# Kernel tuning notes

Hardware: AMD Instinct MI355X
Metric: run time of the kernel (lower is better)

The kernel has to match this reference:

```python
import jax, jax.numpy as jnp
import numpy as np

NUM_HEADS = 12
D = 768
HD = D // NUM_HEADS  # 64

def setup_inputs() -> dict:
    key = jax.random.key(0)
    ks = jax.random.split(key, 9)
    s = 0.02
    return {
        "x": jax.random.normal(ks[0], (4, 2048, D), dtype=jnp.float32),
        "QW_w": jax.random.normal(ks[1], (D, D), dtype=jnp.float32) * s,
        "QW_b": jax.random.normal(ks[2], (D,), dtype=jnp.float32) * s,
        "KW_w": jax.random.normal(ks[3], (D, D), dtype=jnp.float32) * s,
        "KW_b": jax.random.normal(ks[4], (D,), dtype=jnp.float32) * s,
        "VW_w": jax.random.normal(ks[5], (D, D), dtype=jnp.float32) * s,
        "VW_b": jax.random.normal(ks[6], (D,), dtype=jnp.float32) * s,
        "OW_w": jax.random.normal(ks[7], (D, D), dtype=jnp.float32) * s,
        "OW_b": jax.random.normal(ks[8], (D,), dtype=jnp.float32) * s,
    }

def reference(x, QW_w, QW_b, KW_w, KW_b, VW_w, VW_b, OW_w, OW_b):
    b, s, _ = x.shape
    # torch nn.Linear: y = x @ W.T + b
    def proj(w, bias):
        y = jnp.einsum('bsd,ed->bse', x, w) + bias
        return y.reshape(b, s, NUM_HEADS, HD).transpose(0, 2, 1, 3)  # [b,h,s,hd]
    q = proj(QW_w, QW_b)
    k = proj(KW_w, KW_b)
    v = proj(VW_w, VW_b)
    scores = jnp.einsum('bhqd,bhkd->bhqk', q, k) / jnp.sqrt(jnp.float32(HD))
    attn = jax.nn.softmax(scores, axis=-1)
    out = jnp.einsum('bhqk,bhkd->bhqd', attn, v)
    out = out.transpose(0, 2, 1, 3).reshape(b, s, NUM_HEADS * HD)
    return jnp.einsum('bsd,ed->bse', out, OW_w) + OW_b
```

## Files before the change

kernel.cpp:

```cpp
#include <hip/hip_runtime.h>
#include <hip/hip_bf16.h>

#define NH  12
#define HD  64
#define DIM 768
#define SEQ 2048
#define NB  4
#define MM  (NB*SEQ)
#define NKB (SEQ/64)

typedef short    v8s  __attribute__((ext_vector_type(8)));
typedef float    v4f  __attribute__((ext_vector_type(4)));
typedef float    v16f __attribute__((ext_vector_type(16)));
typedef unsigned v4u  __attribute__((ext_vector_type(4)));

#if __has_builtin(__builtin_amdgcn_exp2f)
#define EXP2(x) __builtin_amdgcn_exp2f(x)
#else
#define EXP2(x) __builtin_exp2f(x)
#endif

static __device__ __forceinline__ unsigned short f2b(float f) {
    unsigned int u = __float_as_uint(f);
    return (unsigned short)((u + 0x7FFFu + ((u >> 16) & 1u)) >> 16);
}
static __device__ __forceinline__ unsigned pk2bf(float lo, float hi) {
    return __builtin_amdgcn_perm(__float_as_uint(hi) + 0x8000u,
                                 __float_as_uint(lo) + 0x8000u, 0x07060302u);
}
static __device__ __forceinline__ void g2l16(const unsigned short* g, unsigned short* l) {
    __builtin_amdgcn_global_load_lds(
        (const __attribute__((address_space(1))) void*)g,
        (__attribute__((address_space(3))) void*)l, 16, 0, 0);
}

__global__ void cast_f32_bf16(const float* __restrict__ in,
                              unsigned short* __restrict__ out, int n4) {
    int i = blockIdx.x * blockDim.x + threadIdx.x;
    if (i < n4) {
        float4 v = reinterpret_cast<const float4*>(in)[i];
        ushort4 o;
        o.x = f2b(v.x); o.y = f2b(v.y); o.z = f2b(v.z); o.w = f2b(v.w);
        reinterpret_cast<ushort4*>(out)[i] = o;
    }
}

__global__ void cast4_f32_bf16(const float* __restrict__ i0, const float* __restrict__ i1,
                               const float* __restrict__ i2, const float* __restrict__ i3,
                               unsigned short* __restrict__ o0, unsigned short* __restrict__ o1,
                               unsigned short* __restrict__ o2, unsigned short* __restrict__ o3,
                               int n4) {
    int i = blockIdx.x * blockDim.x + threadIdx.x;
    if (i >= n4) return;
    const float* in; unsigned short* out;
    switch (blockIdx.y) {
        case 0: in = i0; out = o0; break;
        case 1: in = i1; out = o1; break;
        case 2: in = i2; out = o2; break;
        default: in = i3; out = o3; break;
    }
    float4 v = reinterpret_cast<const float4*>(in)[i];
    ushort4 o;
    o.x = f2b(v.x); o.y = f2b(v.y); o.z = f2b(v.z); o.w = f2b(v.w);
    reinterpret_cast<ushort4*>(out)[i] = o;
}

__global__ __launch_bounds__(256, 3) void gemm_qkv(
    const unsigned short* __restrict__ A,
    const unsigned short* __restrict__ Wq,
    const unsigned short* __restrict__ Wk,
    const unsigned short* __restrict__ Wv,
    const float* __restrict__ bq,
    const float* __restrict__ bk,
    const float* __restrict__ bvp,
    unsigned short* __restrict__ Qb,
    unsigned short* __restrict__ Kb,
    unsigned short* __restrict__ Vf)
{
    __shared__ __align__(16) unsigned short As[128 * 64];
    __shared__ __align__(16) unsigned short Bs[3][64 * 64];

    const int tid  = threadIdx.x;
    const int w    = tid >> 6, lane = tid & 63;
    const int quad = lane >> 4, l16 = lane & 15;
    const int wm   = w & 1,  wn = w >> 1;
    const int lane8 = lane >> 3, sc = lane & 7;
    const int m0   = blockIdx.x * 128;
    const int h    = blockIdx.y;
    const int n0   = h * 64;

    v4f acc[3][4][2];
    #pragma unroll
    for (int s = 0; s < 3; ++s)
        #pragma unroll
        for (int i = 0; i < 4; ++i)
            #pragma unroll
            for (int j = 0; j < 2; ++j)
                acc[s][i][j] = v4f{0.f, 0.f, 0.f, 0.f};

    for (int kb = 0; kb < DIM; kb += 64) {
        __syncthreads();
        #pragma unroll
        for (int t = 0; t < 4; ++t) {
            int r8 = w * 32 + t * 8;
            int r  = r8 + lane8;
            int gch = sc ^ (r & 7);
            g2l16(&A[(size_t)(m0 + r) * DIM + kb + gch * 8], &As[r8 * 64]);
        }
        #pragma unroll
        for (int u = 0; u < 6; ++u) {
            int G = w * 6 + u;
            int set = G >> 3, rg = G & 7;
            int row = rg * 8 + lane8;
            int gch = sc ^ (row & 7);
            const unsigned short* Wp = (set == 0) ? Wq : (set == 1) ? Wk : Wv;
            g2l16(&Wp[(size_t)(n0 + row) * DIM + kb + gch * 8], &Bs[set][rg * 8 * 64]);
        }
        __syncthreads();
        #pragma unroll
        for (int kk = 0; kk < 64; kk += 32) {
            int chb = kk >> 3;
            v8s a[4];
            #pragma unroll
            for (int i = 0; i < 4; ++i) {
                int m = wm * 64 + i * 16 + l16;
                a[i] = *reinterpret_cast<const v8s*>(
                    &As[m * 64 + (((chb + quad) ^ (m & 7)) << 3)]);
            }
            #pragma unroll
            for (int s = 0; s < 3; ++s) {
                v8s b[2];
                #pragma unroll
                for (int j = 0; j < 2; ++j) {
                    int n = wn * 32 + j * 16 + l16;
                    b[j] = *reinterpret_cast<const v8s*>(
                        &Bs[s][n * 64 + (((chb + quad) ^ (n & 7)) << 3)]);
                }
                #pragma unroll
                for (int i = 0; i < 4; ++i)
                    #pragma unroll
                    for (int j = 0; j < 2; ++j)
                        acc[s][i][j] = __builtin_amdgcn_mfma_f32_16x16x32_bf16(
                            a[i], b[j], acc[s][i][j], 0, 0, 0);
            }
        }
    }

    #pragma unroll
    for (int s = 0; s < 2; ++s) {
        unsigned short* out = s ? Kb : Qb;
        const float* bias   = s ? bk : bq;
        const float scale   = s ? 1.0f : 0.1803368801f;
        #pragma unroll
        for (int i = 0; i < 4; ++i) {
            #pragma unroll
            for (int j = 0; j < 2; ++j) {
                int hd = wn * 32 + j * 16 + l16;
                float bias_v = bias[n0 + hd];
                #pragma unroll
                for (int r = 0; r < 4; ++r) {
                    int gm = m0 + wm * 64 + i * 16 + quad * 4 + r;
                    int bb = gm >> 11, sq = gm & (SEQ - 1);
                    out[((size_t)(bb * NH + h) * SEQ + sq) * HD + hd] =
                        f2b((acc[s][i][j][r] + bias_v) * scale);
                }
            }
        }
    }
    #pragma unroll
    for (int i = 0; i < 4; ++i) {
        #pragma unroll
        for (int j = 0; j < 2; ++j) {
            int hd = wn * 32 + j * 16 + l16;
            int hb = hd >> 5, l31v = hd & 31;
            float bias_v = bvp[n0 + hd];
            int gm0 = m0 + wm * 64 + i * 16 + quad * 4;
            int bb = gm0 >> 11, sk = gm0 & (SEQ - 1);
            int kbi = sk >> 6;
            int halfv = quad >> 1, j0 = (quad & 1) * 4;
            ushort4 pkv;
            pkv.x = f2b(acc[2][i][j][0] + bias_v);
            pkv.y = f2b(acc[2][i][j][1] + bias_v);
            pkv.z = f2b(acc[2][i][j][2] + bias_v);
            pkv.w = f2b(acc[2][i][j][3] + bias_v);
            size_t frag = ((size_t)(bb * NH + h) * NKB + kbi) * 8 + hb * 4 + i;
            *reinterpret_cast<ushort4*>(
                &Vf[frag * 512 + (halfv * 32 + l31v) * 8 + j0]) = pkv;
        }
    }
}

__global__ __launch_bounds__(256, 3) void gemm_o(
    const unsigned short* __restrict__ A,
    const unsigned short* __restrict__ W,
    const float* __restrict__ bias,
    float* __restrict__ out)
{
    __shared__ __align__(16) unsigned short As[128 * 64];
    __shared__ __align__(16) unsigned short Bs[64 * 64];

    const int tid  = threadIdx.x;
    const int w    = tid >> 6, lane = tid & 63;
    const int quad = lane >> 4, l16 = lane & 15;
    const int wm   = w & 1,  wn = w >> 1;
    const int lane8 = lane >> 3, sc = lane & 7;
    const int m0  = blockIdx.x * 128;
    const int n0l = blockIdx.y * 64;

    v4f acc[4][2];
    #pragma unroll
    for (int i = 0; i < 4; ++i)
        #pragma unroll
        for (int j = 0; j < 2; ++j)
            acc[i][j] = v4f{0.f, 0.f, 0.f, 0.f};

    for (int kb = 0; kb < DIM; kb += 64) {
        __syncthreads();
        #pragma unroll
        for (int t = 0; t < 4; ++t) {
            int r8 = w * 32 + t * 8;
            int r  = r8 + lane8;
            int gch = sc ^ (r & 7);
            g2l16(&A[(size_t)(m0 + r) * DIM + kb + gch * 8], &As[r8 * 64]);
        }
        #pragma unroll
        for (int t = 0; t < 2; ++t) {
            int r8 = (w * 2 + t) * 8;
            int r  = r8 + lane8;
            int gch = sc ^ (r & 7);
            g2l16(&W[(size_t)(n0l + r) * DIM + kb + gch * 8], &Bs[r8 * 64]);
        }
        __syncthreads();
        #pragma unroll
        for (int kk = 0; kk < 64; kk += 32) {
            v8s a[4], b[2];
            int chb = kk >> 3;
            #pragma unroll
            for (int i = 0; i < 4; ++i) {
                int m = wm * 64 + i * 16 + l16;
                a[i] = *reinterpret_cast<const v8s*>(
                    &As[m * 64 + (((chb + quad) ^ (m & 7)) << 3)]);
            }
            #pragma unroll
            for (int j = 0; j < 2; ++j) {
                int n = wn * 32 + j * 16 + l16;
                b[j] = *reinterpret_cast<const v8s*>(
                    &Bs[n * 64 + (((chb + quad) ^ (n & 7)) << 3)]);
            }
            #pragma unroll
            for (int i = 0; i < 4; ++i)
                #pragma unroll
                for (int j = 0; j < 2; ++j)
                    acc[i][j] = __builtin_amdgcn_mfma_f32_16x16x32_bf16(a[i], b[j], acc[i][j], 0, 0, 0);
        }
    }

    #pragma unroll
    for (int i = 0; i < 4; ++i) {
        #pragma unroll
        for (int j = 0; j < 2; ++j) {
            int gn = n0l + wn * 32 + j * 16 + l16;
            float bias_v = bias[gn];
            #pragma unroll
            for (int r = 0; r < 4; ++r) {
                int gm = m0 + wm * 64 + i * 16 + quad * 4 + r;
                out[(size_t)gm * DIM + gn] = acc[i][j][r] + bias_v;
            }
        }
    }
}

__global__ __launch_bounds__(256, 3) void attn(
    const unsigned short* __restrict__ Q,
    const unsigned short* __restrict__ K,
    const unsigned short* __restrict__ Vf,
    unsigned short* __restrict__ ctx)
{
    __shared__ __align__(16) unsigned short Ks[2][64 * 64];

    const int tid  = threadIdx.x;
    const int w    = tid >> 6, lane = tid & 63;
    const int l31  = lane & 31, half = lane >> 5;
    const int lane8 = lane >> 3, sc = lane & 7;
    const int bh   = blockIdx.y;
    const int b    = bh / NH, h = bh % NH;
    const int q0   = blockIdx.x * 128 + w * 32;

    const unsigned short* Qp = Q  + ((size_t)bh * SEQ + q0) * HD;
    const unsigned short* Kp = K  + (size_t)bh * SEQ * HD;
    const unsigned short* Vh = Vf + (size_t)bh * NKB * 8 * 512 + lane * 8;

    v8s bq[4];
    #pragma unroll
    for (int c = 0; c < 4; ++c)
        bq[c] = *reinterpret_cast<const v8s*>(&Qp[l31 * HD + c * 16 + half * 8]);

    v8s va[2][4];
    #pragma unroll
    for (int hb = 0; hb < 2; ++hb)
        #pragma unroll
        for (int c = 0; c < 4; ++c)
            va[hb][c] = *reinterpret_cast<const v8s*>(&Vh[(hb * 4 + c) * 512]);

    v16f o0, o1, Z;
    #pragma unroll
    for (int i = 0; i < 16; ++i) { o0[i] = 0.f; o1[i] = 0.f; Z[i] = 0.f; }
    float li = 0.f;

    const int rx = l31 & 7;
    int rdoff[4];
    #pragma unroll
    for (int c = 0; c < 4; ++c)
        rdoff[c] = l31 * 64 + (((c * 2 + half) ^ rx) << 3);

    #define STAGE_K(kb_, buf_)                                                       \
        do {                                                                         \
            _Pragma("unroll")                                                        \
            for (int t = 0; t < 2; ++t) {                                            \
                int r8  = (t * 4 + w) * 8;                                           \
                int row = r8 + lane8;                                                \
                int gch = sc ^ (row & 7);                                            \
                g2l16(&Kp[(size_t)((kb_) + row) * HD + gch * 8], &Ks[buf_][r8 * 64]);\
            }                                                                        \
        } while (0)

    STAGE_K(0, 0);

    for (int it = 0; it < NKB; ++it) {
        const int buf = it & 1;
        __syncthreads();
        if (it + 1 < NKB) STAGE_K((it + 1) * 64, buf ^ 1);

        v16f s0, s1;
        {
            v8s ka00 = *reinterpret_cast<const v8s*>(&Ks[buf][rdoff[0]]);
            v8s ka10 = *reinterpret_cast<const v8s*>(&Ks[buf][rdoff[0] + 2048]);
            s0 = __builtin_amdgcn_mfma_f32_32x32x16_bf16(ka00, bq[0], Z, 0, 0, 0);
            s1 = __builtin_amdgcn_mfma_f32_32x32x16_bf16(ka10, bq[0], Z, 0, 0, 0);
            #pragma unroll
            for (int c = 1; c < 4; ++c) {
                v8s k0 = *reinterpret_cast<const v8s*>(&Ks[buf][rdoff[c]]);
                v8s k1 = *reinterpret_cast<const v8s*>(&Ks[buf][rdoff[c] + 2048]);
                s0 = __builtin_amdgcn_mfma_f32_32x32x16_bf16(k0, bq[c], s0, 0, 0, 0);
                s1 = __builtin_amdgcn_mfma_f32_32x32x16_bf16(k1, bq[c], s1, 0, 0, 0);
            }
        }

        unsigned pk[8][2];
        #pragma unroll
        for (int g = 0; g < 4; ++g) {
            float e0 = EXP2(s0[4*g+0]), e1 = EXP2(s0[4*g+1]);
            float e2 = EXP2(s0[4*g+2]), e3 = EXP2(s0[4*g+3]);
            li += (e0 + e1) + (e2 + e3);
            pk[g][0] = pk2bf(e0, e1);
            pk[g][1] = pk2bf(e2, e3);
            float f0 = EXP2(s1[4*g+0]), f1 = EXP2(s1[4*g+1]);
            float f2 = EXP2(s1[4*g+2]), f3 = EXP2(s1[4*g+3]);
            li += (f0 + f1) + (f2 + f3);
            pk[4+g][0] = pk2bf(f0, f1);
            pk[4+g][1] = pk2bf(f2, f3);
        }

        #pragma unroll
        for (int cp = 0; cp < 4; ++cp) {
            unsigned a0 = pk[2*cp][0],   a1 = pk[2*cp][1];
            unsigned b0 = pk[2*cp+1][0], b1 = pk[2*cp+1][1];
            unsigned u0 = half ? a0 : b0;
            unsigned u1 = half ? a1 : b1;
            unsigned x0 = __shfl_xor(u0, 32);
            unsigned x1 = __shfl_xor(u1, 32);
            v4u fw;
            fw.x = half ? x0 : a0;
            fw.y = half ? x1 : a1;
            fw.z = half ? b0 : x0;
            fw.w = half ? b1 : x1;
            v8s pf = __builtin_bit_cast(v8s, fw);
            o0 = __builtin_amdgcn_mfma_f32_32x32x16_bf16(va[0][cp], pf, o0, 0, 0, 0);
            o1 = __builtin_amdgcn_mfma_f32_32x32x16_bf16(va[1][cp], pf, o1, 0, 0, 0);
        }

        if (it + 1 < NKB) {
            const unsigned short* Vn = Vh + (size_t)(it + 1) * 8 * 512;
            #pragma unroll
            for (int hb = 0; hb < 2; ++hb)
                #pragma unroll
                for (int c = 0; c < 4; ++c)
                    va[hb][c] = *reinterpret_cast<const v8s*>(&Vn[(hb * 4 + c) * 512]);
        }
    }
    #undef STAGE_K

    float inv = 1.0f / (li + __shfl_xor(li, 32));

    const int q = q0 + l31;
    size_t base = ((size_t)(b * SEQ + q)) * DIM + h * HD;
    #pragma unroll
    for (int g = 0; g < 4; ++g) {
        int hd0 = 8 * g + 4 * half;
        uint2 u0, u1;
        u0.x = pk2bf(o0[4*g+0] * inv, o0[4*g+1] * inv);
        u0.y = pk2bf(o0[4*g+2] * inv, o0[4*g+3] * inv);
        u1.x = pk2bf(o1[4*g+0] * inv, o1[4*g+1] * inv);
        u1.y = pk2bf(o1[4*g+2] * inv, o1[4*g+3] * inv);
        *reinterpret_cast<uint2*>(&ctx[base + hd0])      = u0;
        *reinterpret_cast<uint2*>(&ctx[base + 32 + hd0]) = u1;
    }
}

extern "C" void kernel_launch(void* const* d_in, const int* in_sizes, int n_in,
                              void* d_out, int out_size, void* d_ws, size_t ws_size,
                              hipStream_t stream) {
    const float* x  = (const float*)d_in[0];
    const float* qw = (const float*)d_in[1]; const float* qb = (const float*)d_in[2];
    const float* kw = (const float*)d_in[3]; const float* kb = (const float*)d_in[4];
    const float* vw = (const float*)d_in[5]; const float* vb = (const float*)d_in[6];
    const float* ow = (const float*)d_in[7]; const float* ob = (const float*)d_in[8];
    float* out = (float*)d_out;

    char* ws = (char*)d_ws;
    size_t off = 0;
    auto alloc = [&](size_t bytes) -> unsigned short* {
        unsigned short* p = (unsigned short*)(ws + off);
        off += (bytes + 255) & ~(size_t)255;
        return p;
    };
    const size_t XB = (size_t)MM * DIM * 2;
    const size_t WB = (size_t)DIM * DIM * 2;
    const size_t QB = (size_t)NB * NH * SEQ * HD * 2;

    unsigned short* xb  = alloc(XB);
    unsigned short* wqb = alloc(WB);
    unsigned short* wkb = alloc(WB);
    unsigned short* wvb = alloc(WB);
    unsigned short* wob = alloc(WB);
    unsigned short* Qb  = alloc(QB);
    unsigned short* Kb  = alloc(QB);
    unsigned short* Vfb = alloc(QB);
    unsigned short* ctx = alloc(XB);

    const int n4x = MM * DIM / 4;
    const int n4w = DIM * DIM / 4;
    cast_f32_bf16<<<(n4x + 255) / 256, 256, 0, stream>>>(x, xb, n4x);
    cast4_f32_bf16<<<dim3((n4w + 255) / 256, 4), 256, 0, stream>>>(
        qw, kw, vw, ow, wqb, wkb, wvb, wob, n4w);

    gemm_qkv<<<dim3(MM / 128, NH), 256, 0, stream>>>(
        xb, wqb, wkb, wvb, qb, kb, vb, Qb, Kb, Vfb);

    attn<<<dim3(SEQ / 128, NB * NH), 256, 0, stream>>>(Qb, Kb, Vfb, ctx);

    gemm_o<<<dim3(MM / 128, DIM / 64), 256, 0, stream>>>(ctx, wob, ob, out);
}
```

Before: 210.8 us.

## Store K in MFMA fragment layout and load K directly to registers

The QKV GEMM now writes K in a pre-swizzled per-64-key-block fragment layout, the same way V is stored. The attention kernel then loads K fragments straight from global memory into registers, prefetching one block ahead, instead of staging K through double-buffered LDS with __syncthreads. This removes the LDS traffic and barriers from the attention loop, at the cost of more register pressure and every wave reading K from global/L2 on its own. The packed bf16 conversion also switches from a manual perm trick to the hardware v_cvt_pk_bf16_f32 instruction.

```diff
diff --git a/kernel.cpp b/kernel.cpp
--- a/kernel.cpp
+++ b/kernel.cpp
@@ -24,9 +24,10 @@
     unsigned int u = __float_as_uint(f);
     return (unsigned short)((u + 0x7FFFu + ((u >> 16) & 1u)) >> 16);
 }
-static __device__ __forceinline__ unsigned pk2bf(float lo, float hi) {
-    return __builtin_amdgcn_perm(__float_as_uint(hi) + 0x8000u,
-                                 __float_as_uint(lo) + 0x8000u, 0x07060302u);
+static __device__ __forceinline__ unsigned cvtpk(float lo, float hi) {
+    unsigned r;
+    asm("v_cvt_pk_bf16_f32 %0, %1, %2" : "=v"(r) : "v"(lo), "v"(hi));
+    return r;
 }
 static __device__ __forceinline__ void g2l16(const unsigned short* g, unsigned short* l) {
     __builtin_amdgcn_global_load_lds(
@@ -74,7 +75,7 @@
     const float* __restrict__ bk,
     const float* __restrict__ bvp,
     unsigned short* __restrict__ Qb,
-    unsigned short* __restrict__ Kb,
+    unsigned short* __restrict__ Kfo,
     unsigned short* __restrict__ Vf)
 {
     __shared__ __align__(16) unsigned short As[128 * 64];
@@ -147,24 +148,39 @@
     }
 
     #pragma unroll
-    for (int s = 0; s < 2; ++s) {
-        unsigned short* out = s ? Kb : Qb;
-        const float* bias   = s ? bk : bq;
-        const float scale   = s ? 1.0f : 0.1803368801f;
-        #pragma unroll
-        for (int i = 0; i < 4; ++i) {
-            #pragma unroll
-            for (int j = 0; j < 2; ++j) {
-                int hd = wn * 32 + j * 16 + l16;
-                float bias_v = bias[n0 + hd];
-                #pragma unroll
-                for (int r = 0; r < 4; ++r) {
-                    int gm = m0 + wm * 64 + i * 16 + quad * 4 + r;
-                    int bb = gm >> 11, sq = gm & (SEQ - 1);
-                    out[((size_t)(bb * NH + h) * SEQ + sq) * HD + hd] =
-                        f2b((acc[s][i][j][r] + bias_v) * scale);
-                }
-            }
+    for (int i = 0; i < 4; ++i) {
+        #pragma unroll
+        for (int j = 0; j < 2; ++j) {
+            int hd = wn * 32 + j * 16 + l16;
+            float bias_v = bq[n0 + hd];
+            #pragma unroll
+            for (int r = 0; r < 4; ++r) {
+                int gm = m0 + wm * 64 + i * 16 + quad * 4 + r;
+                int bb = gm >> 11, sq = gm & (SEQ - 1);
+                Qb[((size_t)(bb * NH + h) * SEQ + sq) * HD + hd] =
+                    f2b((acc[0][i][j][r] + bias_v) * 0.1803368801f);
+            }
+        }
+    }
+    #pragma unroll
+    for (int i = 0; i < 4; ++i) {
+        int kh = i >> 1;
+        #pragma unroll
+        for (int j = 0; j < 2; ++j) {
+            int hd = wn * 32 + j * 16 + l16;
+            int c  = hd >> 4;
+            int half_a = (l16 >> 3) & 1;
+            int jj = l16 & 7;
+            float bias_v = bk[n0 + hd];
+            int gm0 = m0 + wm * 64 + i * 16 + quad * 4;
+            int bb = gm0 >> 11, sk = gm0 & (SEQ - 1);
+            int t = sk >> 6;
+            int l31k = (i & 1) * 16 + quad * 4;
+            size_t frag = ((size_t)(bb * NH + h) * NKB + t) * 8 + kh * 4 + c;
+            unsigned short* dst = &Kfo[frag * 512 + (half_a * 32 + l31k) * 8 + jj];
+            #pragma unroll
+            for (int r = 0; r < 4; ++r)
+                dst[r * 8] = f2b(acc[1][i][j][r] + bias_v);
         }
     }
     #pragma unroll
@@ -272,78 +288,53 @@
 
 __global__ __launch_bounds__(256, 3) void attn(
     const unsigned short* __restrict__ Q,
-    const unsigned short* __restrict__ K,
+    const unsigned short* __restrict__ Kf,
     const unsigned short* __restrict__ Vf,
     unsigned short* __restrict__ ctx)
 {
-    __shared__ __align__(16) unsigned short Ks[2][64 * 64];
-
     const int tid  = threadIdx.x;
     const int w    = tid >> 6, lane = tid & 63;
     const int l31  = lane & 31, half = lane >> 5;
-    const int lane8 = lane >> 3, sc = lane & 7;
     const int bh   = blockIdx.y;
     const int b    = bh / NH, h = bh % NH;
     const int q0   = blockIdx.x * 128 + w * 32;
 
     const unsigned short* Qp = Q  + ((size_t)bh * SEQ + q0) * HD;
-    const unsigned short* Kp = K  + (size_t)bh * SEQ * HD;
-    const unsigned short* Vh = Vf + (size_t)bh * NKB * 8 * 512 + lane * 8;
+    const unsigned short* Vh = Vf + (size_t)bh * (NKB * 8 * 512) + lane * 8;
+    const unsigned short* Kh = Kf + (size_t)bh * (NKB * 8 * 512) + lane * 8;
 
     v8s bq[4];
     #pragma unroll
     for (int c = 0; c < 4; ++c)
         bq[c] = *reinterpret_cast<const v8s*>(&Qp[l31 * HD + c * 16 + half * 8]);
 
-    v8s va[2][4];
-    #pragma unroll
-    for (int hb = 0; hb < 2; ++hb)
-        #pragma unroll
-        for (int c = 0; c < 4; ++c)
-            va[hb][c] = *reinterpret_cast<const v8s*>(&Vh[(hb * 4 + c) * 512]);
+    v8s ka[2][4], va[2][4];
+    #pragma unroll
+    for (int g = 0; g < 8; ++g)
+        reinterpret_cast<v8s*>(ka)[g] = *reinterpret_cast<const v8s*>(&Kh[g * 512]);
+    #pragma unroll
+    for (int g = 0; g < 8; ++g)
+        reinterpret_cast<v8s*>(va)[g] = *reinterpret_cast<const v8s*>(&Vh[g * 512]);
 
     v16f o0, o1, Z;
     #pragma unroll
     for (int i = 0; i < 16; ++i) { o0[i] = 0.f; o1[i] = 0.f; Z[i] = 0.f; }
     float li = 0.f;
 
-    const int rx = l31 & 7;
-    int rdoff[4];
-    #pragma unroll
-    for (int c = 0; c < 4; ++c)
-        rdoff[c] = l31 * 64 + (((c * 2 + half) ^ rx) << 3);
-
-    #define STAGE_K(kb_, buf_)                                                       \
-        do {                                                                         \
-            _Pragma("unroll")                                                        \
-            for (int t = 0; t < 2; ++t) {                                            \
-                int r8  = (t * 4 + w) * 8;                                           \
-                int row = r8 + lane8;                                                \
-                int gch = sc ^ (row & 7);                                            \
-                g2l16(&Kp[(size_t)((kb_) + row) * HD + gch * 8], &Ks[buf_][r8 * 64]);\
-            }                                                                        \
-        } while (0)
-
-    STAGE_K(0, 0);
-
     for (int it = 0; it < NKB; ++it) {
-        const int buf = it & 1;
-        __syncthreads();
-        if (it + 1 < NKB) STAGE_K((it + 1) * 64, buf ^ 1);
-
-        v16f s0, s1;
+        v16f s0 = __builtin_amdgcn_mfma_f32_32x32x16_bf16(ka[0][0], bq[0], Z, 0, 0, 0);
+        v16f s1 = __builtin_amdgcn_mfma_f32_32x32x16_bf16(ka[1][0], bq[0], Z, 0, 0, 0);
+        #pragma unroll
+        for (int c = 1; c < 4; ++c) {
+            s0 = __builtin_amdgcn_mfma_f32_32x32x16_bf16(ka[0][c], bq[c], s0, 0, 0, 0);
+            s1 = __builtin_amdgcn_mfma_f32_32x32x16_bf16(ka[1][c], bq[c], s1, 0, 0, 0);
+        }
+
         {
-            v8s ka00 = *reinterpret_cast<const v8s*>(&Ks[buf][rdoff[0]]);
-            v8s ka10 = *reinterpret_cast<const v8s*>(&Ks[buf][rdoff[0] + 2048]);
-            s0 = __builtin_amdgcn_mfma_f32_32x32x16_bf16(ka00, bq[0], Z, 0, 0, 0);
-            s1 = __builtin_amdgcn_mfma_f32_32x32x16_bf16(ka10, bq[0], Z, 0, 0, 0);
-            #pragma unroll
-            for (int c = 1; c < 4; ++c) {
-                v8s k0 = *reinterpret_cast<const v8s*>(&Ks[buf][rdoff[c]]);
-                v8s k1 = *reinterpret_cast<const v8s*>(&Ks[buf][rdoff[c] + 2048]);
-                s0 = __builtin_amdgcn_mfma_f32_32x32x16_bf16(k0, bq[c], s0, 0, 0, 0);
-                s1 = __builtin_amdgcn_mfma_f32_32x32x16_bf16(k1, bq[c], s1, 0, 0, 0);
-            }
+            const unsigned short* Kn = Kh + (size_t)(it + 1 < NKB ? it + 1 : it) * (8 * 512);
+            #pragma unroll
+            for (int g = 0; g < 8; ++g)
+                reinterpret_cast<v8s*>(ka)[g] = *reinterpret_cast<const v8s*>(&Kn[g * 512]);
         }
 
         unsigned pk[8][2];
@@ -352,13 +343,13 @@
             float e0 = EXP2(s0[4*g+0]), e1 = EXP2(s0[4*g+1]);
             float e2 = EXP2(s0[4*g+2]), e3 = EXP2(s0[4*g+3]);
             li += (e0 + e1) + (e2 + e3);
-            pk[g][0] = pk2bf(e0, e1);
-            pk[g][1] = pk2bf(e2, e3);
+            pk[g][0] = cvtpk(e0, e1);
+            pk[g][1] = cvtpk(e2, e3);
             float f0 = EXP2(s1[4*g+0]), f1 = EXP2(s1[4*g+1]);
             float f2 = EXP2(s1[4*g+2]), f3 = EXP2(s1[4*g+3]);
             li += (f0 + f1) + (f2 + f3);
-            pk[4+g][0] = pk2bf(f0, f1);
-            pk[4+g][1] = pk2bf(f2, f3);
+            pk[4+g][0] = cvtpk(f0, f1);
+            pk[4+g][1] = cvtpk(f2, f3);
         }
 
         #pragma unroll
@@ -379,16 +370,13 @@
             o1 = __builtin_amdgcn_mfma_f32_32x32x16_bf16(va[1][cp], pf, o1, 0, 0, 0);
         }
 
-        if (it + 1 < NKB) {
-            const unsigned short* Vn = Vh + (size_t)(it + 1) * 8 * 512;
-            #pragma unroll
-            for (int hb = 0; hb < 2; ++hb)
-                #pragma unroll
-                for (int c = 0; c < 4; ++c)
-                    va[hb][c] = *reinterpret_cast<const v8s*>(&Vn[(hb * 4 + c) * 512]);
-        }
-    }
-    #undef STAGE_K
+        {
+            const unsigned short* Vn = Vh + (size_t)(it + 1 < NKB ? it + 1 : it) * (8 * 512);
+            #pragma unroll
+            for (int g = 0; g < 8; ++g)
+                reinterpret_cast<v8s*>(va)[g] = *reinterpret_cast<const v8s*>(&Vn[g * 512]);
+        }
+    }
 
     float inv = 1.0f / (li + __shfl_xor(li, 32));
 
@@ -398,10 +386,10 @@
     for (int g = 0; g < 4; ++g) {
         int hd0 = 8 * g + 4 * half;
         uint2 u0, u1;
-        u0.x = pk2bf(o0[4*g+0] * inv, o0[4*g+1] * inv);
-        u0.y = pk2bf(o0[4*g+2] * inv, o0[4*g+3] * inv);
-        u1.x = pk2bf(o1[4*g+0] * inv, o1[4*g+1] * inv);
-        u1.y = pk2bf(o1[4*g+2] * inv, o1[4*g+3] * inv);
+        u0.x = cvtpk(o0[4*g+0] * inv, o0[4*g+1] * inv);
+        u0.y = cvtpk(o0[4*g+2] * inv, o0[4*g+3] * inv);
+        u1.x = cvtpk(o1[4*g+0] * inv, o1[4*g+1] * inv);
+        u1.y = cvtpk(o1[4*g+2] * inv, o1[4*g+3] * inv);
         *reinterpret_cast<uint2*>(&ctx[base + hd0])      = u0;
         *reinterpret_cast<uint2*>(&ctx[base + 32 + hd0]) = u1;
     }
@@ -434,7 +422,7 @@
     unsigned short* wvb = alloc(WB);
     unsigned short* wob = alloc(WB);
     unsigned short* Qb  = alloc(QB);
-    unsigned short* Kb  = alloc(QB);
+    unsigned short* Kfb = alloc(QB);
     unsigned short* Vfb = alloc(QB);
     unsigned short* ctx = alloc(XB);
 
@@ -445,9 +433,9 @@
         qw, kw, vw, ow, wqb, wkb, wvb, wob, n4w);
 
     gemm_qkv<<<dim3(MM / 128, NH), 256, 0, stream>>>(
-        xb, wqb, wkb, wvb, qb, kb, vb, Qb, Kb, Vfb);
-
-    attn<<<dim3(SEQ / 128, NB * NH), 256, 0, stream>>>(Qb, Kb, Vfb, ctx);
+        xb, wqb, wkb, wvb, qb, kb, vb, Qb, Kfb, Vfb);
+
+    attn<<<dim3(SEQ / 128, NB * NH), 256, 0, stream>>>(Qb, Kfb, Vfb, ctx);
 
     gemm_o<<<dim3(MM / 128, DIM / 64), 256, 0, stream>>>(ctx, wob, ob, out);
 }
```

Result: slower. 241.5 us (+14.6%).
